# Kernel optimization log

Measured on AMD Instinct MI355X. Metric: run time of the kernel, lower is better.

Reference implementation:

```python
import jax, jax.numpy as jnp
import numpy as np

NEG_INF = -1e9  # masked_fill value in torch code
HELP_THRESH = -1e8  # help_scores > -1e8 marks valid dependency entries


def setup_inputs() -> dict:
    key = jax.random.key(0)
    ks = jax.random.split(key, 16)
    B, S, D, H, DK = 8, 512, 1024, 16, 64
    sc = 0.02
    x = jax.random.normal(ks[0], (B, S, D), jnp.float32)
    Wq = jax.random.normal(ks[1], (D, H * DK), jnp.float32) * sc
    bq = jax.random.normal(ks[2], (H * DK,), jnp.float32) * sc
    Wk = jax.random.normal(ks[3], (D, H * DK), jnp.float32) * sc
    bk = jax.random.normal(ks[4], (H * DK,), jnp.float32) * sc
    Wv = jax.random.normal(ks[5], (D, H * DK), jnp.float32) * sc
    bv = jax.random.normal(ks[6], (H * DK,), jnp.float32) * sc
    Wo = jax.random.normal(ks[7], (H * DK, D), jnp.float32) * sc
    bo = jax.random.normal(ks[8], (D,), jnp.float32) * sc
    ln_g = jnp.ones((D,), jnp.float32)
    ln_b = jnp.zeros((D,), jnp.float32)
    help_vals = jax.random.normal(ks[9], (B, H, S, S), jnp.float32)
    help_mask = jax.random.randint(ks[10], (B, H, S, S), 0, 2).astype(jnp.int32)
    attn_mask = jax.random.randint(ks[11], (B, S, S), 0, 2).astype(bool)
    return {"x": x, "Wq": Wq, "bq": bq, "Wk": Wk, "bk": bk, "Wv": Wv,
            "bv": bv, "Wo": Wo, "bo": bo, "ln_g": ln_g, "ln_b": ln_b,
            "help_vals": help_vals, "help_mask": help_mask, "attn_mask": attn_mask}


def reference(x, Wq, bq, Wk, bk, Wv, bv, Wo, bo, ln_g, ln_b,
              help_vals, help_mask, attn_mask):
    B, S, D = x.shape
    H, DK = 16, 64
    # projections -> [B,H,S,dk]
    q = (x @ Wq + bq).reshape(B, S, H, DK).transpose(0, 2, 1, 3)
    k = (x @ Wk + bk).reshape(B, S, H, DK).transpose(0, 2, 1, 3)
    v = (x @ Wv + bv).reshape(B, S, H, DK).transpose(0, 2, 1, 3)
    scores = jnp.einsum('bhqd,bhkd->bhqk', q, k) / np.sqrt(DK).astype(np.float32)
    scores = jnp.where(attn_mask[:, None, :, :], NEG_INF, scores)
    # dependency-tree score blending (ScaledDotProductAttention)
    help_scores = jnp.where(help_mask.astype(bool), help_vals, NEG_INF)
    m = (help_scores > HELP_THRESH).astype(scores.dtype)
    dep_w = m * 0.5
    seq_w = m * 0.5 + (1.0 - m)
    scores = help_scores * dep_w + scores * seq_w
    attn = jax.nn.softmax(scores, axis=-1)
    ctx = jnp.einsum('bhqk,bhkd->bhqd', attn, v)  # [B,H,S,dv]
    ctx = ctx.transpose(0, 2, 1, 3).reshape(B, S, H * DK)
    out = ctx @ Wo + bo
    # residual + LayerNorm (input_dim == output_dim path)
    y = out + x
    mu = y.mean(-1, keepdims=True)
    var = ((y - mu) ** 2).mean(-1, keepdims=True)
    y = (y - mu) / jnp.sqrt(var + 1e-5) * ln_g + ln_b
    return y, attn
```

## Files before the change

kernel.cpp:

```cpp
#include <hip/hip_runtime.h>
#include <hip/hip_bf16.h>

typedef __bf16 bf16_t;
typedef __bf16 bf16x4 __attribute__((ext_vector_type(4)));
typedef __bf16 bf16x8 __attribute__((ext_vector_type(8)));
typedef float f32x4 __attribute__((ext_vector_type(4)));


__device__ __forceinline__ f32x4 mfma16(bf16x8 a, bf16x8 b, f32x4 c) {
    return __builtin_amdgcn_mfma_f32_16x16x32_bf16(a, b, c, 0, 0, 0);
}

__device__ __forceinline__ float blendf(float s, int am, int hm, float hv) {
    s = am ? -1e9f : s;
    return hm ? 0.5f * hv + 0.5f * s : s;
}

__global__ __launch_bounds__(256) void cast_kernel(const float* __restrict__ x,
                                                   bf16_t* __restrict__ xb) {
    size_t i = ((size_t)blockIdx.x * 256 + threadIdx.x) * 4;
    float4 v = *(const float4*)(x + i);
    bf16x4 o;
    o[0] = (bf16_t)v.x; o[1] = (bf16_t)v.y; o[2] = (bf16_t)v.z; o[3] = (bf16_t)v.w;
    *(bf16x4*)(xb + i) = o;
}

__global__ __launch_bounds__(256) void transpose_kernel(const float* __restrict__ W,
                                                        bf16_t* __restrict__ Wt) {
    __shared__ float tile[32][33];
    int tx = threadIdx.x & 31, ty = threadIdx.x >> 5;
    int bx = blockIdx.x * 32, by = blockIdx.y * 32;
#pragma unroll
    for (int j = 0; j < 4; j++)
        tile[ty + j * 8][tx] = W[(size_t)(by + ty + j * 8) * 1024 + bx + tx];
    __syncthreads();
#pragma unroll
    for (int j = 0; j < 4; j++)
        Wt[(size_t)(bx + ty + j * 8) * 1024 + by + tx] = (bf16_t)tile[tx][ty + j * 8];
}

template <int MODE>
__global__ __launch_bounds__(256) void gemm_bt(const bf16_t* __restrict__ A,
                                               const bf16_t* __restrict__ Bt,
                                               const float* __restrict__ bias,
                                               const float* __restrict__ resid,
                                               void* __restrict__ outp) {
    constexpr int K = 1024, N = 1024;
    __shared__ bf16_t As[128][40];
    __shared__ bf16_t Bs[128][40];
    const int t = threadIdx.x;
    const int lane = t & 63;
    const int wv = t >> 6;
    const int lm = lane & 15, q4 = lane >> 4;
    const int mblk = blockIdx.y * 128, nblk = blockIdx.x * 128;
    const int mrow = (wv & 1) * 64, ncol = (wv >> 1) * 64;

    f32x4 acc[4][4];
#pragma unroll
    for (int r = 0; r < 4; r++)
#pragma unroll
        for (int c = 0; c < 4; c++) acc[r][c] = (f32x4){0.f, 0.f, 0.f, 0.f};

    for (int k0 = 0; k0 < K; k0 += 32) {
#pragma unroll
        for (int ld = 0; ld < 2; ld++) {
            int id = t + ld * 256;
            int r = id >> 2, c = (id & 3) * 8;
            *(bf16x8*)&As[r][c] = *(const bf16x8*)&A[(size_t)(mblk + r) * K + k0 + c];
            *(bf16x8*)&Bs[r][c] = *(const bf16x8*)&Bt[(size_t)(nblk + r) * K + k0 + c];
        }
        __syncthreads();
        bf16x8 af[4], bf[4];
#pragma unroll
        for (int r = 0; r < 4; r++) af[r] = *(const bf16x8*)&As[mrow + r * 16 + lm][q4 * 8];
#pragma unroll
        for (int c = 0; c < 4; c++) bf[c] = *(const bf16x8*)&Bs[ncol + c * 16 + lm][q4 * 8];
#pragma unroll
        for (int r = 0; r < 4; r++)
#pragma unroll
            for (int c = 0; c < 4; c++) acc[r][c] = mfma16(af[r], bf[c], acc[r][c]);
        __syncthreads();
    }

#pragma unroll
    for (int r = 0; r < 4; r++)
#pragma unroll
        for (int c = 0; c < 4; c++)
#pragma unroll
            for (int i = 0; i < 4; i++) {
                int m = mblk + mrow + r * 16 + q4 * 4 + i;
                int n = nblk + ncol + c * 16 + lm;
                float v = acc[r][c][i] + bias[n];
                if (MODE == 0) {
                    int b = m >> 9, s = m & 511, h = n >> 6, d = n & 63;
                    ((bf16_t*)outp)[(((size_t)(b * 16 + h) * 512) + s) * 64 + d] = (bf16_t)v;
                } else if (MODE == 2) {
                    int b = m >> 9, s = m & 511, h = n >> 6, d = n & 63;
                    ((bf16_t*)outp)[(((size_t)(b * 16 + h) * 64) + d) * 512 + s] = (bf16_t)v;
                } else {
                    ((float*)outp)[(size_t)m * N + n] = v + resid[(size_t)m * N + n];
                }
            }
}

__global__ __launch_bounds__(256) void attn_fused_kernel(const bf16_t* __restrict__ Qb,
                                                         const bf16_t* __restrict__ Kb,
                                                         const bf16_t* __restrict__ Vt,
                                                         const float* __restrict__ help_vals,
                                                         const int* __restrict__ help_mask,
                                                         const int* __restrict__ attn_mask,
                                                         float* __restrict__ attn_out,
                                                         bf16_t* __restrict__ xo) {
    const int t = threadIdx.x;
    const int lane = t & 63, wv = t >> 6;
    const int lm = lane & 15, q4 = lane >> 4;
    const int bh = blockIdx.y;
    const int b = bh >> 4, h = bh & 15;
    const int q0 = blockIdx.x * 16;
    const bf16_t* Qp = Qb + (size_t)bh * 512 * 64;
    const bf16_t* Kp = Kb + (size_t)bh * 512 * 64;
    const bf16_t* Vp = Vt + (size_t)bh * 64 * 512;

    __shared__ float S[16][532];
    __shared__ bf16_t Pl[16][552];

    const bf16x8 bq0 = *(const bf16x8*)&Qp[(size_t)(q0 + lm) * 64 + q4 * 8];
    const bf16x8 bq1 = *(const bf16x8*)&Qp[(size_t)(q0 + lm) * 64 + 32 + q4 * 8];

    f32x4 acc[8];
#pragma unroll
    for (int kt = 0; kt < 8; kt++) acc[kt] = (f32x4){0.f, 0.f, 0.f, 0.f};
#pragma unroll
    for (int kt = 0; kt < 8; kt++) {
        const int krow = wv * 128 + kt * 16 + lm;
        bf16x8 ak0 = *(const bf16x8*)&Kp[(size_t)krow * 64 + q4 * 8];
        bf16x8 ak1 = *(const bf16x8*)&Kp[(size_t)krow * 64 + 32 + q4 * 8];
        acc[kt] = mfma16(ak0, bq0, acc[kt]);
        acc[kt] = mfma16(ak1, bq1, acc[kt]);
    }
#pragma unroll
    for (int kt = 0; kt < 8; kt++) {
        f32x4 sv = acc[kt] * 0.125f;
        *(f32x4*)&S[lm][wv * 128 + kt * 16 + q4 * 4] = sv;
    }
    __syncthreads();

#pragma unroll 2
    for (int rr = 0; rr < 4; rr++) {
        const int r = wv * 4 + rr;
        const int q = q0 + r;
        const size_t qrow = ((size_t)bh * 512 + q) * 512;
        const size_t arow = ((size_t)b * 512 + q) * 512;
        const int c0 = lane * 4;
        const int c1 = 256 + lane * 4;
        f32x4 s0 = *(const f32x4*)&S[r][c0];
        f32x4 s1 = *(const f32x4*)&S[r][c1];
        const float4 hv0 = *(const float4*)&help_vals[qrow + c0];
        const float4 hv1 = *(const float4*)&help_vals[qrow + c1];
        const int4 hm0 = *(const int4*)&help_mask[qrow + c0];
        const int4 hm1 = *(const int4*)&help_mask[qrow + c1];
        const int4 am0 = *(const int4*)&attn_mask[arow + c0];
        const int4 am1 = *(const int4*)&attn_mask[arow + c1];
        float s[8];
        s[0] = blendf(s0[0], am0.x, hm0.x, hv0.x);
        s[1] = blendf(s0[1], am0.y, hm0.y, hv0.y);
        s[2] = blendf(s0[2], am0.z, hm0.z, hv0.z);
        s[3] = blendf(s0[3], am0.w, hm0.w, hv0.w);
        s[4] = blendf(s1[0], am1.x, hm1.x, hv1.x);
        s[5] = blendf(s1[1], am1.y, hm1.y, hv1.y);
        s[6] = blendf(s1[2], am1.z, hm1.z, hv1.z);
        s[7] = blendf(s1[3], am1.w, hm1.w, hv1.w);
        float mloc = fmaxf(fmaxf(fmaxf(s[0], s[1]), fmaxf(s[2], s[3])),
                           fmaxf(fmaxf(s[4], s[5]), fmaxf(s[6], s[7])));
#pragma unroll
        for (int off = 1; off < 64; off <<= 1) mloc = fmaxf(mloc, __shfl_xor(mloc, off));
        float lsum = 0.f;
#pragma unroll
        for (int i = 0; i < 8; i++) {
            s[i] = __expf(s[i] - mloc);
            lsum += s[i];
        }
#pragma unroll
        for (int off = 1; off < 64; off <<= 1) lsum += __shfl_xor(lsum, off);
        const float rinv = 1.0f / lsum;
        float4 o0, o1;
        o0.x = s[0] * rinv; o0.y = s[1] * rinv; o0.z = s[2] * rinv; o0.w = s[3] * rinv;
        o1.x = s[4] * rinv; o1.y = s[5] * rinv; o1.z = s[6] * rinv; o1.w = s[7] * rinv;
        *(float4*)&attn_out[qrow + c0] = o0;
        *(float4*)&attn_out[qrow + c1] = o1;
        bf16x4 p0, p1;
        p0[0] = (bf16_t)o0.x; p0[1] = (bf16_t)o0.y; p0[2] = (bf16_t)o0.z; p0[3] = (bf16_t)o0.w;
        p1[0] = (bf16_t)o1.x; p1[1] = (bf16_t)o1.y; p1[2] = (bf16_t)o1.z; p1[3] = (bf16_t)o1.w;
        *(bf16x4*)&Pl[r][c0] = p0;
        *(bf16x4*)&Pl[r][c1] = p1;
    }
    __syncthreads();

    f32x4 acc2[4];
#pragma unroll
    for (int mt = 0; mt < 4; mt++) acc2[mt] = (f32x4){0.f, 0.f, 0.f, 0.f};
    const int kb0 = wv * 128;
#pragma unroll
    for (int C = 0; C < 4; C++) {
        const bf16x8 pf = *(const bf16x8*)&Pl[lm][kb0 + C * 32 + q4 * 8];
#pragma unroll
        for (int mt = 0; mt < 4; mt++) {
            const bf16x8 vf =
                *(const bf16x8*)&Vp[(size_t)(mt * 16 + lm) * 512 + kb0 + C * 32 + q4 * 8];
            acc2[mt] = mfma16(vf, pf, acc2[mt]);
        }
    }

    float* redp = &S[0][0];
#pragma unroll
    for (int mt = 0; mt < 4; mt++)
        *(f32x4*)(redp + ((wv * 16 + lm) * 68 + mt * 16 + q4 * 4)) = acc2[mt];
    __syncthreads();
    {
        const int qq = t >> 4;
        const int d4 = (t & 15) * 4;
        f32x4 r0 = *(const f32x4*)(redp + ((0 * 16 + qq) * 68 + d4));
        f32x4 r1 = *(const f32x4*)(redp + ((1 * 16 + qq) * 68 + d4));
        f32x4 r2 = *(const f32x4*)(redp + ((2 * 16 + qq) * 68 + d4));
        f32x4 r3 = *(const f32x4*)(redp + ((3 * 16 + qq) * 68 + d4));
        f32x4 sum = r0 + r1 + r2 + r3;
        bf16x4 o;
        o[0] = (bf16_t)sum[0]; o[1] = (bf16_t)sum[1];
        o[2] = (bf16_t)sum[2]; o[3] = (bf16_t)sum[3];
        *(bf16x4*)&xo[((size_t)(b * 512 + q0 + qq)) * 1024 + h * 64 + d4] = o;
    }
}

__global__ __launch_bounds__(256) void layernorm_kernel(const float* __restrict__ ypre,
                                                        const float* __restrict__ g,
                                                        const float* __restrict__ bvec,
                                                        float* __restrict__ out) {
    int row = blockIdx.x;
    int t = threadIdx.x;
    float4 v = ((const float4*)(ypre + (size_t)row * 1024))[t];
    float s = v.x + v.y + v.z + v.w;
    float sq = v.x * v.x + v.y * v.y + v.z * v.z + v.w * v.w;
#pragma unroll
    for (int off = 32; off; off >>= 1) {
        s += __shfl_down(s, off);
        sq += __shfl_down(sq, off);
    }
    __shared__ float ss[4], ssq[4];
    if ((t & 63) == 0) { ss[t >> 6] = s; ssq[t >> 6] = sq; }
    __syncthreads();
    float tot = ss[0] + ss[1] + ss[2] + ss[3];
    float totq = ssq[0] + ssq[1] + ssq[2] + ssq[3];
    float mu = tot * (1.0f / 1024.0f);
    float var = totq * (1.0f / 1024.0f) - mu * mu;
    float rstd = rsqrtf(var + 1e-5f);
    float4 gg = ((const float4*)g)[t];
    float4 bb = ((const float4*)bvec)[t];
    float4 o;
    o.x = (v.x - mu) * rstd * gg.x + bb.x;
    o.y = (v.y - mu) * rstd * gg.y + bb.y;
    o.z = (v.z - mu) * rstd * gg.z + bb.z;
    o.w = (v.w - mu) * rstd * gg.w + bb.w;
    ((float4*)(out + (size_t)row * 1024))[t] = o;
}

extern "C" void kernel_launch(void* const* d_in, const int* in_sizes, int n_in,
                              void* d_out, int out_size, void* d_ws, size_t ws_size,
                              hipStream_t stream) {
    const float* x         = (const float*)d_in[0];
    const float* Wq        = (const float*)d_in[1];
    const float* bq        = (const float*)d_in[2];
    const float* Wk        = (const float*)d_in[3];
    const float* bk        = (const float*)d_in[4];
    const float* Wv        = (const float*)d_in[5];
    const float* bv        = (const float*)d_in[6];
    const float* Wo        = (const float*)d_in[7];
    const float* bo        = (const float*)d_in[8];
    const float* ln_g      = (const float*)d_in[9];
    const float* ln_b      = (const float*)d_in[10];
    const float* help_vals = (const float*)d_in[11];
    const int*   help_mask = (const int*)d_in[12];
    const int*   attn_mask = (const int*)d_in[13];

    char* ws = (char*)d_ws;
    bf16_t* xb   = (bf16_t*)(ws);
    bf16_t* wqt  = (bf16_t*)(ws + ((size_t)8 << 20));
    bf16_t* wkt  = (bf16_t*)(ws + ((size_t)10 << 20));
    bf16_t* wvt  = (bf16_t*)(ws + ((size_t)12 << 20));
    bf16_t* wot  = (bf16_t*)(ws + ((size_t)14 << 20));
    bf16_t* qb   = (bf16_t*)(ws + ((size_t)16 << 20));
    bf16_t* kb   = (bf16_t*)(ws + ((size_t)24 << 20));
    bf16_t* vt   = (bf16_t*)(ws + ((size_t)32 << 20));
    bf16_t* xo   = (bf16_t*)(ws + ((size_t)40 << 20));
    float*  ypre = (float*)(ws + ((size_t)48 << 20));

    float* y_out = (float*)d_out;
    float* attn_out = y_out + (size_t)4096 * 1024;

    cast_kernel<<<4096, 256, 0, stream>>>(x, xb);
    dim3 tg(32, 32);
    transpose_kernel<<<tg, 256, 0, stream>>>(Wq, wqt);
    transpose_kernel<<<tg, 256, 0, stream>>>(Wk, wkt);
    transpose_kernel<<<tg, 256, 0, stream>>>(Wv, wvt);
    transpose_kernel<<<tg, 256, 0, stream>>>(Wo, wot);

    dim3 gg(8, 32);
    gemm_bt<0><<<gg, 256, 0, stream>>>(xb, wqt, bq, nullptr, qb);
    gemm_bt<0><<<gg, 256, 0, stream>>>(xb, wkt, bk, nullptr, kb);
    gemm_bt<2><<<gg, 256, 0, stream>>>(xb, wvt, bv, nullptr, vt);

    dim3 ga(32, 128);
    attn_fused_kernel<<<ga, 256, 0, stream>>>(qb, kb, vt, help_vals, help_mask, attn_mask,
                                              attn_out, xo);

    gemm_bt<3><<<gg, 256, 0, stream>>>(xo, wot, bo, x, ypre);
    layernorm_kernel<<<4096, 256, 0, stream>>>(ypre, ln_g, ln_b, y_out);
}
```

Before: 536.6 us.

## Batch QKV/transpose launches, double-buffer GEMMs with direct LDS loads, prefetch mask rows

Merges the four weight transposes and the three QKV projections into single launches that use a z grid index. The GEMMs now double-buffer their shared-memory tiles and fill them with global_load_lds, which overlaps loading the next K slice with the MFMA work on the current one. The attention kernel prefetches the next row's help/attn mask values with nontemporal loads and uses nontemporal stores for attn_out. It drops the separate bf16 P buffer in favour of reusing S, and adds setprio hints and occupancy launch bounds. These changes target launch overhead, memory latency and LDS footprint, at the cost of extra conversions and higher register pressure.

```diff
diff --git a/kernel.cpp b/kernel.cpp
--- a/kernel.cpp
+++ b/kernel.cpp
@@ -5,6 +5,7 @@
 typedef __bf16 bf16x4 __attribute__((ext_vector_type(4)));
 typedef __bf16 bf16x8 __attribute__((ext_vector_type(8)));
 typedef float f32x4 __attribute__((ext_vector_type(4)));
+typedef int i32x4 __attribute__((ext_vector_type(4)));
 
 
 __device__ __forceinline__ f32x4 mfma16(bf16x8 a, bf16x8 b, f32x4 c) {
@@ -15,6 +16,11 @@
     s = am ? -1e9f : s;
     return hm ? 0.5f * hv + 0.5f * s : s;
 }
+
+#define GLOAD_LDS16(g, l)                                                   \
+    __builtin_amdgcn_global_load_lds(                                       \
+        (const __attribute__((address_space(1))) void*)(g),                 \
+        (__attribute__((address_space(3))) void*)(l), 16, 0, 0)
 
 __global__ __launch_bounds__(256) void cast_kernel(const float* __restrict__ x,
                                                    bf16_t* __restrict__ xb) {
@@ -25,9 +31,15 @@
     *(bf16x4*)(xb + i) = o;
 }
 
-__global__ __launch_bounds__(256) void transpose_kernel(const float* __restrict__ W,
-                                                        bf16_t* __restrict__ Wt) {
+__global__ __launch_bounds__(256) void transpose_kernel(const float* __restrict__ Wq,
+                                                        const float* __restrict__ Wk,
+                                                        const float* __restrict__ Wv,
+                                                        const float* __restrict__ Wo,
+                                                        bf16_t* __restrict__ Wt_base) {
     __shared__ float tile[32][33];
+    const int z = blockIdx.z;
+    const float* W = (z == 0) ? Wq : (z == 1) ? Wk : (z == 2) ? Wv : Wo;
+    bf16_t* Wt = Wt_base + ((size_t)z << 20);
     int tx = threadIdx.x & 31, ty = threadIdx.x >> 5;
     int bx = blockIdx.x * 32, by = blockIdx.y * 32;
 #pragma unroll
@@ -39,21 +51,26 @@
         Wt[(size_t)(bx + ty + j * 8) * 1024 + by + tx] = (bf16_t)tile[tx][ty + j * 8];
 }
 
-template <int MODE>
-__global__ __launch_bounds__(256) void gemm_bt(const bf16_t* __restrict__ A,
-                                               const bf16_t* __restrict__ Bt,
-                                               const float* __restrict__ bias,
-                                               const float* __restrict__ resid,
-                                               void* __restrict__ outp) {
-    constexpr int K = 1024, N = 1024;
-    __shared__ bf16_t As[128][40];
-    __shared__ bf16_t Bs[128][40];
+__global__ __launch_bounds__(256, 4) void gemm_qkv(const bf16_t* __restrict__ A,
+                                                   const bf16_t* __restrict__ WtB,
+                                                   const float* __restrict__ bq,
+                                                   const float* __restrict__ bk,
+                                                   const float* __restrict__ bv,
+                                                   bf16_t* __restrict__ qb,
+                                                   bf16_t* __restrict__ kb,
+                                                   bf16_t* __restrict__ vt) {
+    constexpr int K = 1024;
+    __shared__ bf16_t As[2][128][32];
+    __shared__ bf16_t Bs[2][128][32];
+    const int z = blockIdx.z;
+    const bf16_t* Bt = WtB + ((size_t)z << 20);
+    const float* bias = (z == 0) ? bq : (z == 1) ? bk : bv;
     const int t = threadIdx.x;
-    const int lane = t & 63;
-    const int wv = t >> 6;
+    const int lane = t & 63, wv = t >> 6;
     const int lm = lane & 15, q4 = lane >> 4;
     const int mblk = blockIdx.y * 128, nblk = blockIdx.x * 128;
     const int mrow = (wv & 1) * 64, ncol = (wv >> 1) * 64;
+    const int sr = t >> 2, sc = (t & 3) * 8;
 
     f32x4 acc[4][4];
 #pragma unroll
@@ -61,25 +78,35 @@
 #pragma unroll
         for (int c = 0; c < 4; c++) acc[r][c] = (f32x4){0.f, 0.f, 0.f, 0.f};
 
+    const bf16_t* ga = &A[(size_t)(mblk + sr) * K + sc];
+    const bf16_t* gb = &Bt[(size_t)(nblk + sr) * K + sc];
+    GLOAD_LDS16(ga, &As[0][sr][sc]);
+    GLOAD_LDS16(ga + (size_t)64 * K, &As[0][sr + 64][sc]);
+    GLOAD_LDS16(gb, &Bs[0][sr][sc]);
+    GLOAD_LDS16(gb + (size_t)64 * K, &Bs[0][sr + 64][sc]);
+    __syncthreads();
+
+    int cur = 0;
     for (int k0 = 0; k0 < K; k0 += 32) {
-#pragma unroll
-        for (int ld = 0; ld < 2; ld++) {
-            int id = t + ld * 256;
-            int r = id >> 2, c = (id & 3) * 8;
-            *(bf16x8*)&As[r][c] = *(const bf16x8*)&A[(size_t)(mblk + r) * K + k0 + c];
-            *(bf16x8*)&Bs[r][c] = *(const bf16x8*)&Bt[(size_t)(nblk + r) * K + k0 + c];
+        if (k0 + 32 < K) {
+            const bf16_t* ga2 = ga + k0 + 32;
+            const bf16_t* gb2 = gb + k0 + 32;
+            GLOAD_LDS16(ga2, &As[cur ^ 1][sr][sc]);
+            GLOAD_LDS16(ga2 + (size_t)64 * K, &As[cur ^ 1][sr + 64][sc]);
+            GLOAD_LDS16(gb2, &Bs[cur ^ 1][sr][sc]);
+            GLOAD_LDS16(gb2 + (size_t)64 * K, &Bs[cur ^ 1][sr + 64][sc]);
         }
+        bf16x8 af[4], bfr[4];
+#pragma unroll
+        for (int r = 0; r < 4; r++) af[r] = *(const bf16x8*)&As[cur][mrow + r * 16 + lm][q4 * 8];
+#pragma unroll
+        for (int c = 0; c < 4; c++) bfr[c] = *(const bf16x8*)&Bs[cur][ncol + c * 16 + lm][q4 * 8];
+#pragma unroll
+        for (int r = 0; r < 4; r++)
+#pragma unroll
+            for (int c = 0; c < 4; c++) acc[r][c] = mfma16(af[r], bfr[c], acc[r][c]);
         __syncthreads();
-        bf16x8 af[4], bf[4];
-#pragma unroll
-        for (int r = 0; r < 4; r++) af[r] = *(const bf16x8*)&As[mrow + r * 16 + lm][q4 * 8];
-#pragma unroll
-        for (int c = 0; c < 4; c++) bf[c] = *(const bf16x8*)&Bs[ncol + c * 16 + lm][q4 * 8];
-#pragma unroll
-        for (int r = 0; r < 4; r++)
-#pragma unroll
-            for (int c = 0; c < 4; c++) acc[r][c] = mfma16(af[r], bf[c], acc[r][c]);
-        __syncthreads();
+        cur ^= 1;
     }
 
 #pragma unroll
@@ -91,26 +118,90 @@
                 int m = mblk + mrow + r * 16 + q4 * 4 + i;
                 int n = nblk + ncol + c * 16 + lm;
                 float v = acc[r][c][i] + bias[n];
-                if (MODE == 0) {
-                    int b = m >> 9, s = m & 511, h = n >> 6, d = n & 63;
-                    ((bf16_t*)outp)[(((size_t)(b * 16 + h) * 512) + s) * 64 + d] = (bf16_t)v;
-                } else if (MODE == 2) {
-                    int b = m >> 9, s = m & 511, h = n >> 6, d = n & 63;
-                    ((bf16_t*)outp)[(((size_t)(b * 16 + h) * 64) + d) * 512 + s] = (bf16_t)v;
+                int b = m >> 9, s = m & 511, h = n >> 6, d = n & 63;
+                if (z < 2) {
+                    bf16_t* o = z ? kb : qb;
+                    o[(((size_t)(b * 16 + h) * 512) + s) * 64 + d] = (bf16_t)v;
                 } else {
-                    ((float*)outp)[(size_t)m * N + n] = v + resid[(size_t)m * N + n];
+                    vt[(((size_t)(b * 16 + h) * 64) + d) * 512 + s] = (bf16_t)v;
                 }
             }
 }
 
-__global__ __launch_bounds__(256) void attn_fused_kernel(const bf16_t* __restrict__ Qb,
-                                                         const bf16_t* __restrict__ Kb,
-                                                         const bf16_t* __restrict__ Vt,
-                                                         const float* __restrict__ help_vals,
-                                                         const int* __restrict__ help_mask,
-                                                         const int* __restrict__ attn_mask,
-                                                         float* __restrict__ attn_out,
-                                                         bf16_t* __restrict__ xo) {
+__global__ __launch_bounds__(256, 4) void gemm_out(const bf16_t* __restrict__ A,
+                                                   const bf16_t* __restrict__ Bt,
+                                                   const float* __restrict__ bias,
+                                                   const float* __restrict__ resid,
+                                                   float* __restrict__ outp) {
+    constexpr int K = 1024, N = 1024;
+    __shared__ bf16_t As[2][128][32];
+    __shared__ bf16_t Bs[2][128][32];
+    const int t = threadIdx.x;
+    const int lane = t & 63, wv = t >> 6;
+    const int lm = lane & 15, q4 = lane >> 4;
+    const int mblk = blockIdx.y * 128, nblk = blockIdx.x * 128;
+    const int mrow = (wv & 1) * 64, ncol = (wv >> 1) * 64;
+    const int sr = t >> 2, sc = (t & 3) * 8;
+
+    f32x4 acc[4][4];
+#pragma unroll
+    for (int r = 0; r < 4; r++)
+#pragma unroll
+        for (int c = 0; c < 4; c++) acc[r][c] = (f32x4){0.f, 0.f, 0.f, 0.f};
+
+    const bf16_t* ga = &A[(size_t)(mblk + sr) * K + sc];
+    const bf16_t* gb = &Bt[(size_t)(nblk + sr) * K + sc];
+    GLOAD_LDS16(ga, &As[0][sr][sc]);
+    GLOAD_LDS16(ga + (size_t)64 * K, &As[0][sr + 64][sc]);
+    GLOAD_LDS16(gb, &Bs[0][sr][sc]);
+    GLOAD_LDS16(gb + (size_t)64 * K, &Bs[0][sr + 64][sc]);
+    __syncthreads();
+
+    int cur = 0;
+    for (int k0 = 0; k0 < K; k0 += 32) {
+        if (k0 + 32 < K) {
+            const bf16_t* ga2 = ga + k0 + 32;
+            const bf16_t* gb2 = gb + k0 + 32;
+            GLOAD_LDS16(ga2, &As[cur ^ 1][sr][sc]);
+            GLOAD_LDS16(ga2 + (size_t)64 * K, &As[cur ^ 1][sr + 64][sc]);
+            GLOAD_LDS16(gb2, &Bs[cur ^ 1][sr][sc]);
+            GLOAD_LDS16(gb2 + (size_t)64 * K, &Bs[cur ^ 1][sr + 64][sc]);
+        }
+        bf16x8 af[4], bfr[4];
+#pragma unroll
+        for (int r = 0; r < 4; r++) af[r] = *(const bf16x8*)&As[cur][mrow + r * 16 + lm][q4 * 8];
+#pragma unroll
+        for (int c = 0; c < 4; c++) bfr[c] = *(const bf16x8*)&Bs[cur][ncol + c * 16 + lm][q4 * 8];
+#pragma unroll
+        for (int r = 0; r < 4; r++)
+#pragma unroll
+            for (int c = 0; c < 4; c++) acc[r][c] = mfma16(af[r], bfr[c], acc[r][c]);
+        __syncthreads();
+        cur ^= 1;
+    }
+
+#pragma unroll
+    for (int r = 0; r < 4; r++)
+#pragma unroll
+        for (int c = 0; c < 4; c++)
+#pragma unroll
+            for (int i = 0; i < 4; i++) {
+                int m = mblk + mrow + r * 16 + q4 * 4 + i;
+                int n = nblk + ncol + c * 16 + lm;
+                float v = acc[r][c][i] + bias[n];
+                outp[(size_t)m * N + n] = v + resid[(size_t)m * N + n];
+            }
+}
+
+__global__ __launch_bounds__(256, 4) void attn_fused_kernel(const bf16_t* __restrict__ Qb,
+                                                            const bf16_t* __restrict__ Kb,
+                                                            const bf16_t* __restrict__ Vt,
+                                                            const float* __restrict__ help_vals,
+                                                            const int* __restrict__ help_mask,
+                                                            const int* __restrict__ attn_mask,
+                                                            float* __restrict__ attn_out,
+                                                            bf16_t* __restrict__ xo) {
+    constexpr int SS = 516;
     const int t = threadIdx.x;
     const int lane = t & 63, wv = t >> 6;
     const int lm = lane & 15, q4 = lane >> 4;
@@ -121,15 +212,28 @@
     const bf16_t* Kp = Kb + (size_t)bh * 512 * 64;
     const bf16_t* Vp = Vt + (size_t)bh * 64 * 512;
 
-    __shared__ float S[16][532];
-    __shared__ bf16_t Pl[16][552];
+    __shared__ float S[16][SS];
+
+    const int c0 = lane * 4, c1 = 256 + lane * 4;
+    const int rbase = wv * 4;
+    const size_t qrow0 = ((size_t)bh * 512 + q0 + rbase) * 512;
+    const size_t arow0 = ((size_t)b * 512 + q0 + rbase) * 512;
+
+    f32x4 hv[2][2];
+    i32x4 hm[2][2], am[2][2];
+    hv[0][0] = __builtin_nontemporal_load((const f32x4*)&help_vals[qrow0 + c0]);
+    hv[0][1] = __builtin_nontemporal_load((const f32x4*)&help_vals[qrow0 + c1]);
+    hm[0][0] = __builtin_nontemporal_load((const i32x4*)&help_mask[qrow0 + c0]);
+    hm[0][1] = __builtin_nontemporal_load((const i32x4*)&help_mask[qrow0 + c1]);
+    am[0][0] = *(const i32x4*)&attn_mask[arow0 + c0];
+    am[0][1] = *(const i32x4*)&attn_mask[arow0 + c1];
 
     const bf16x8 bq0 = *(const bf16x8*)&Qp[(size_t)(q0 + lm) * 64 + q4 * 8];
     const bf16x8 bq1 = *(const bf16x8*)&Qp[(size_t)(q0 + lm) * 64 + 32 + q4 * 8];
-
     f32x4 acc[8];
 #pragma unroll
     for (int kt = 0; kt < 8; kt++) acc[kt] = (f32x4){0.f, 0.f, 0.f, 0.f};
+    __builtin_amdgcn_s_setprio(1);
 #pragma unroll
     for (int kt = 0; kt < 8; kt++) {
         const int krow = wv * 128 + kt * 16 + lm;
@@ -138,61 +242,55 @@
         acc[kt] = mfma16(ak0, bq0, acc[kt]);
         acc[kt] = mfma16(ak1, bq1, acc[kt]);
     }
-#pragma unroll
-    for (int kt = 0; kt < 8; kt++) {
-        f32x4 sv = acc[kt] * 0.125f;
-        *(f32x4*)&S[lm][wv * 128 + kt * 16 + q4 * 4] = sv;
-    }
-    __syncthreads();
-
-#pragma unroll 2
+    __builtin_amdgcn_s_setprio(0);
+#pragma unroll
+    for (int kt = 0; kt < 8; kt++)
+        *(f32x4*)&S[lm][wv * 128 + kt * 16 + q4 * 4] = acc[kt] * 0.125f;
+    __syncthreads();
+
+#pragma unroll
     for (int rr = 0; rr < 4; rr++) {
-        const int r = wv * 4 + rr;
-        const int q = q0 + r;
-        const size_t qrow = ((size_t)bh * 512 + q) * 512;
-        const size_t arow = ((size_t)b * 512 + q) * 512;
-        const int c0 = lane * 4;
-        const int c1 = 256 + lane * 4;
+        const int sl = rr & 1, sn = sl ^ 1;
+        if (rr < 3) {
+            const size_t qr = qrow0 + (size_t)(rr + 1) * 512;
+            const size_t ar = arow0 + (size_t)(rr + 1) * 512;
+            hv[sn][0] = __builtin_nontemporal_load((const f32x4*)&help_vals[qr + c0]);
+            hv[sn][1] = __builtin_nontemporal_load((const f32x4*)&help_vals[qr + c1]);
+            hm[sn][0] = __builtin_nontemporal_load((const i32x4*)&help_mask[qr + c0]);
+            hm[sn][1] = __builtin_nontemporal_load((const i32x4*)&help_mask[qr + c1]);
+            am[sn][0] = *(const i32x4*)&attn_mask[ar + c0];
+            am[sn][1] = *(const i32x4*)&attn_mask[ar + c1];
+        }
+        const int r = rbase + rr;
+        const size_t qrow = qrow0 + (size_t)rr * 512;
         f32x4 s0 = *(const f32x4*)&S[r][c0];
         f32x4 s1 = *(const f32x4*)&S[r][c1];
-        const float4 hv0 = *(const float4*)&help_vals[qrow + c0];
-        const float4 hv1 = *(const float4*)&help_vals[qrow + c1];
-        const int4 hm0 = *(const int4*)&help_mask[qrow + c0];
-        const int4 hm1 = *(const int4*)&help_mask[qrow + c1];
-        const int4 am0 = *(const int4*)&attn_mask[arow + c0];
-        const int4 am1 = *(const int4*)&attn_mask[arow + c1];
-        float s[8];
-        s[0] = blendf(s0[0], am0.x, hm0.x, hv0.x);
-        s[1] = blendf(s0[1], am0.y, hm0.y, hv0.y);
-        s[2] = blendf(s0[2], am0.z, hm0.z, hv0.z);
-        s[3] = blendf(s0[3], am0.w, hm0.w, hv0.w);
-        s[4] = blendf(s1[0], am1.x, hm1.x, hv1.x);
-        s[5] = blendf(s1[1], am1.y, hm1.y, hv1.y);
-        s[6] = blendf(s1[2], am1.z, hm1.z, hv1.z);
-        s[7] = blendf(s1[3], am1.w, hm1.w, hv1.w);
-        float mloc = fmaxf(fmaxf(fmaxf(s[0], s[1]), fmaxf(s[2], s[3])),
-                           fmaxf(fmaxf(s[4], s[5]), fmaxf(s[6], s[7])));
+        float sv[8];
+#pragma unroll
+        for (int i = 0; i < 4; i++) sv[i] = blendf(s0[i], am[sl][0][i], hm[sl][0][i], hv[sl][0][i]);
+#pragma unroll
+        for (int i = 0; i < 4; i++)
+            sv[4 + i] = blendf(s1[i], am[sl][1][i], hm[sl][1][i], hv[sl][1][i]);
+        float mloc = fmaxf(fmaxf(fmaxf(sv[0], sv[1]), fmaxf(sv[2], sv[3])),
+                           fmaxf(fmaxf(sv[4], sv[5]), fmaxf(sv[6], sv[7])));
 #pragma unroll
         for (int off = 1; off < 64; off <<= 1) mloc = fmaxf(mloc, __shfl_xor(mloc, off));
         float lsum = 0.f;
 #pragma unroll
         for (int i = 0; i < 8; i++) {
-            s[i] = __expf(s[i] - mloc);
-            lsum += s[i];
+            sv[i] = __expf(sv[i] - mloc);
+            lsum += sv[i];
         }
 #pragma unroll
         for (int off = 1; off < 64; off <<= 1) lsum += __shfl_xor(lsum, off);
         const float rinv = 1.0f / lsum;
-        float4 o0, o1;
-        o0.x = s[0] * rinv; o0.y = s[1] * rinv; o0.z = s[2] * rinv; o0.w = s[3] * rinv;
-        o1.x = s[4] * rinv; o1.y = s[5] * rinv; o1.z = s[6] * rinv; o1.w = s[7] * rinv;
-        *(float4*)&attn_out[qrow + c0] = o0;
-        *(float4*)&attn_out[qrow + c1] = o1;
-        bf16x4 p0, p1;
-        p0[0] = (bf16_t)o0.x; p0[1] = (bf16_t)o0.y; p0[2] = (bf16_t)o0.z; p0[3] = (bf16_t)o0.w;
-        p1[0] = (bf16_t)o1.x; p1[1] = (bf16_t)o1.y; p1[2] = (bf16_t)o1.z; p1[3] = (bf16_t)o1.w;
-        *(bf16x4*)&Pl[r][c0] = p0;
-        *(bf16x4*)&Pl[r][c1] = p1;
+        f32x4 o0, o1;
+        o0[0] = sv[0] * rinv; o0[1] = sv[1] * rinv; o0[2] = sv[2] * rinv; o0[3] = sv[3] * rinv;
+        o1[0] = sv[4] * rinv; o1[1] = sv[5] * rinv; o1[2] = sv[6] * rinv; o1[3] = sv[7] * rinv;
+        *(f32x4*)&S[r][c0] = o0;
+        *(f32x4*)&S[r][c1] = o1;
+        __builtin_nontemporal_store(o0, (f32x4*)&attn_out[qrow + c0]);
+        __builtin_nontemporal_store(o1, (f32x4*)&attn_out[qrow + c1]);
     }
     __syncthreads();
 
@@ -200,9 +298,14 @@
 #pragma unroll
     for (int mt = 0; mt < 4; mt++) acc2[mt] = (f32x4){0.f, 0.f, 0.f, 0.f};
     const int kb0 = wv * 128;
+    __builtin_amdgcn_s_setprio(1);
 #pragma unroll
     for (int C = 0; C < 4; C++) {
-        const bf16x8 pf = *(const bf16x8*)&Pl[lm][kb0 + C * 32 + q4 * 8];
+        f32x4 pa = *(const f32x4*)&S[lm][kb0 + C * 32 + q4 * 8];
+        f32x4 pb = *(const f32x4*)&S[lm][kb0 + C * 32 + q4 * 8 + 4];
+        bf16x8 pf;
+        pf[0] = (bf16_t)pa[0]; pf[1] = (bf16_t)pa[1]; pf[2] = (bf16_t)pa[2]; pf[3] = (bf16_t)pa[3];
+        pf[4] = (bf16_t)pb[0]; pf[5] = (bf16_t)pb[1]; pf[6] = (bf16_t)pb[2]; pf[7] = (bf16_t)pb[3];
 #pragma unroll
         for (int mt = 0; mt < 4; mt++) {
             const bf16x8 vf =
@@ -210,6 +313,8 @@
             acc2[mt] = mfma16(vf, pf, acc2[mt]);
         }
     }
+    __builtin_amdgcn_s_setprio(0);
+    __syncthreads();
 
     float* redp = &S[0][0];
 #pragma unroll
@@ -284,8 +389,6 @@
     char* ws = (char*)d_ws;
     bf16_t* xb   = (bf16_t*)(ws);
     bf16_t* wqt  = (bf16_t*)(ws + ((size_t)8 << 20));
-    bf16_t* wkt  = (bf16_t*)(ws + ((size_t)10 << 20));
-    bf16_t* wvt  = (bf16_t*)(ws + ((size_t)12 << 20));
     bf16_t* wot  = (bf16_t*)(ws + ((size_t)14 << 20));
     bf16_t* qb   = (bf16_t*)(ws + ((size_t)16 << 20));
     bf16_t* kb   = (bf16_t*)(ws + ((size_t)24 << 20));
@@ -297,21 +400,13 @@
     float* attn_out = y_out + (size_t)4096 * 1024;
 
     cast_kernel<<<4096, 256, 0, stream>>>(x, xb);
-    dim3 tg(32, 32);
-    transpose_kernel<<<tg, 256, 0, stream>>>(Wq, wqt);
-    transpose_kernel<<<tg, 256, 0, stream>>>(Wk, wkt);
-    transpose_kernel<<<tg, 256, 0, stream>>>(Wv, wvt);
-    transpose_kernel<<<tg, 256, 0, stream>>>(Wo, wot);
-
-    dim3 gg(8, 32);
-    gemm_bt<0><<<gg, 256, 0, stream>>>(xb, wqt, bq, nullptr, qb);
-    gemm_bt<0><<<gg, 256, 0, stream>>>(xb, wkt, bk, nullptr, kb);
-    gemm_bt<2><<<gg, 256, 0, stream>>>(xb, wvt, bv, nullptr, vt);
-
-    dim3 ga(32, 128);
-    attn_fused_kernel<<<ga, 256, 0, stream>>>(qb, kb, vt, help_vals, help_mask, attn_mask,
-                                              attn_out, xo);
-
-    gemm_bt<3><<<gg, 256, 0, stream>>>(xo, wot, bo, x, ypre);
+    transpose_kernel<<<dim3(32, 32, 4), 256, 0, stream>>>(Wq, Wk, Wv, Wo, wqt);
+
+    gemm_qkv<<<dim3(8, 32, 3), 256, 0, stream>>>(xb, wqt, bq, bk, bv, qb, kb, vt);
+
+    attn_fused_kernel<<<dim3(32, 128), 256, 0, stream>>>(qb, kb, vt, help_vals, help_mask,
+                                                         attn_mask, attn_out, xo);
+
+    gemm_out<<<dim3(8, 32), 256, 0, stream>>>(xo, wot, bo, x, ypre);
     layernorm_kernel<<<4096, 256, 0, stream>>>(ypre, ln_g, ln_b, y_out);
 }
```

Result: faster. 478.2 us (-10.9%).
